# Kernel tuning notes

Hardware: AMD Instinct MI355X
Metric: run time of the kernel (lower is better)

Reference implementation:

```python
import jax, jax.numpy as jnp
import numpy as np


def setup_inputs() -> dict:
    key = jax.random.key(0)
    ks = jax.random.split(key, 5)
    B, DEC, ENC, H = 4, 256, 256, 512  # feature_dim = hl_size = 512, mlp hidden = 512
    decoder_states = jax.random.normal(ks[0], (B, DEC, H), dtype=jnp.float32)
    encoder_states = jax.random.normal(ks[1], (B, ENC, H), dtype=jnp.float32)
    ext_mask = jnp.zeros((B, DEC, ENC), dtype=bool)  # self.mask set externally; all-False here
    W_mlp = jax.random.normal(ks[2], (2 * H, H), dtype=jnp.float32) * 0.02  # Linear(2H -> H)
    b_mlp = jnp.zeros((H,), dtype=jnp.float32)
    W_out = jax.random.normal(ks[3], (H, 1), dtype=jnp.float32) * 0.02  # Linear(H -> 1)
    b_out = jnp.zeros((1,), dtype=jnp.float32)
    return {"decoder_states": decoder_states, "encoder_states": encoder_states,
            "ext_mask": ext_mask, "W_mlp": W_mlp, "b_mlp": b_mlp,
            "W_out": W_out, "b_out": b_out}


def reference(decoder_states, encoder_states, ext_mask, W_mlp, b_mlp, W_out, b_out):
    # decoder_states: [B, dec, H]; encoder_states: [B, enc, H]
    H = encoder_states.shape[-1]
    # pad mask: positions where encoder feature-0 equals 0.0 -> [B, 1, enc]
    pad_mask = (encoder_states == 0.0)[:, :, :1]
    pad_mask = jnp.swapaxes(pad_mask, 1, 2)  # [B, 1, enc]
    # cat(enc, dec) @ W_mlp  ==  enc @ W_mlp[:H] + dec @ W_mlp[H:]  (avoids 2H concat)
    enc_proj = jnp.einsum('beh,hm->bem', encoder_states, W_mlp[:H])   # [B, enc, Hm]
    dec_proj = jnp.einsum('bdh,hm->bdm', decoder_states, W_mlp[H:])   # [B, dec, Hm]
    hidden = jnp.tanh(dec_proj[:, :, None, :] + enc_proj[:, None, :, :] + b_mlp)  # [B, dec, enc, Hm]
    attn = jnp.einsum('bdem,mo->bde', hidden, W_out) + b_out[0]       # [B, dec, enc]
    attn = jnp.where(ext_mask, -jnp.inf, attn)
    attn = jnp.where(pad_mask, -jnp.inf, attn)
    attn = jax.nn.softmax(attn, axis=-1)
    context = jnp.einsum('bde,beh->bdh', attn, encoder_states)        # [B, dec, H]
    return (context, attn)
```

## Files before the change

### kernel.cpp

```cpp
#include <hip/hip_runtime.h>
#include <math.h>

#define B 4
#define DEC 256
#define ENC 256
#define HDIM 512

#define TANH_SCALE 2.8853900817779268f
#define LOG2E 1.4426950408889634f

__device__ __forceinline__ float fast_exp2(float x) { return __builtin_amdgcn_exp2f(x); }
__device__ __forceinline__ float fast_rcp(float x)  { return __builtin_amdgcn_rcpf(x); }

typedef __attribute__((ext_vector_type(8))) short bf16x8;
typedef __attribute__((ext_vector_type(4))) short bf16x4;
typedef __attribute__((ext_vector_type(4))) float f32x4;

__device__ __forceinline__ unsigned short bf16_rne(float x) {
    unsigned u = __float_as_uint(x);
    return (unsigned short)((u + 0x7FFFu + ((u >> 16) & 1u)) >> 16);
}
__device__ __forceinline__ float bf16_to_f(unsigned short h) {
    return __uint_as_float((unsigned)h << 16);
}

#define W_OFS(m, k) ((((long)(m) >> 4) << 13) + (((long)(k) >> 3) << 7) + (((m) & 15) << 3) + ((k) & 7))

__global__ __launch_bounds__(256) void convert_kernel(
    const float* __restrict__ enc, const float* __restrict__ dec,
    const float* __restrict__ Wmlp,
    unsigned short* __restrict__ Xh_e, unsigned short* __restrict__ Xl_e,
    unsigned short* __restrict__ Xh_d, unsigned short* __restrict__ Xl_d,
    unsigned short* __restrict__ Wh_e, unsigned short* __restrict__ Wl_e,
    unsigned short* __restrict__ Wh_d, unsigned short* __restrict__ Wl_d)
{
    const int tid = threadIdx.x, z = blockIdx.z;
    if (z < 2) {
        const float* X = z ? dec : enc;
        unsigned short* H = z ? Xh_d : Xh_e;
        unsigned short* L = z ? Xl_d : Xl_e;
        const long i8 = ((long)blockIdx.x * 256 + tid) * 8;
        float4 v0 = *(const float4*)(X + i8);
        float4 v1 = *(const float4*)(X + i8 + 4);
        float xs[8] = {v0.x, v0.y, v0.z, v0.w, v1.x, v1.y, v1.z, v1.w};
        bf16x8 hv, lv;
#pragma unroll
        for (int j = 0; j < 8; ++j) {
            unsigned short h = bf16_rne(xs[j]);
            hv[j] = (short)h;
            lv[j] = (short)bf16_rne(xs[j] - bf16_to_f(h));
        }
        *(bf16x8*)(H + i8) = hv;
        *(bf16x8*)(L + i8) = lv;
    } else {
        const float* Wsrc = Wmlp + (z == 3 ? (long)HDIM * HDIM : 0);
        unsigned short* H = (z == 3) ? Wh_d : Wh_e;
        unsigned short* L = (z == 3) ? Wl_d : Wl_e;
        const int t = blockIdx.x * 256 + tid;
        const int m = t & 511;
        const int k0 = (t >> 9) << 2;
        bf16x4 hv, lv;
#pragma unroll
        for (int j = 0; j < 4; ++j) {
            float x = Wsrc[(long)(k0 + j) * 512 + m];
            unsigned short h = bf16_rne(x);
            hv[j] = (short)h;
            lv[j] = (short)bf16_rne(x - bf16_to_f(h));
        }
        const long ofs = W_OFS(m, k0);
        *(bf16x4*)(H + ofs) = hv;
        *(bf16x4*)(L + ofs) = lv;
    }
}

__global__ __launch_bounds__(256) void proj_mfma_kernel(
    const unsigned short* __restrict__ Xh_e, const unsigned short* __restrict__ Xl_e,
    const unsigned short* __restrict__ Xh_d, const unsigned short* __restrict__ Xl_d,
    const unsigned short* __restrict__ Wh_e, const unsigned short* __restrict__ Wl_e,
    const unsigned short* __restrict__ Wh_d, const unsigned short* __restrict__ Wl_d,
    const float* __restrict__ bmlp,
    float* __restrict__ ET, float* __restrict__ Dmat)
{
    const int tid = threadIdx.x;
    const int wave = tid >> 6, lane = tid & 63;
    const int z = blockIdx.z;
    const int r0w = blockIdx.x * 64 + wave * 16;
    const int m0 = blockIdx.y * 32;
    const unsigned short* Xh = z ? Xh_d : Xh_e;
    const unsigned short* Xl = z ? Xl_d : Xl_e;
    const unsigned short* Wh = z ? Wh_d : Wh_e;
    const unsigned short* Wl = z ? Wl_d : Wl_e;

    const int col = lane & 15;
    const int quad = lane >> 4;

    const unsigned short* pah = Xh + (long)(r0w + col) * 512 + quad * 8;
    const unsigned short* pal = Xl + (long)(r0w + col) * 512 + quad * 8;
    const long bofs = ((long)(m0 >> 4) << 13) + (quad << 7) + (col << 3);
    const unsigned short* pb0h = Wh + bofs;
    const unsigned short* pb0l = Wl + bofs;
    const unsigned short* pb1h = Wh + bofs + 8192;
    const unsigned short* pb1l = Wl + bofs + 8192;

    f32x4 a0h = {0.f,0.f,0.f,0.f}, a0x = {0.f,0.f,0.f,0.f};
    f32x4 a1h = {0.f,0.f,0.f,0.f}, a1x = {0.f,0.f,0.f,0.f};

    bf16x8 Ah = *(const bf16x8*)pah,  Al = *(const bf16x8*)pal;
    bf16x8 B0h = *(const bf16x8*)pb0h, B0l = *(const bf16x8*)pb0l;
    bf16x8 B1h = *(const bf16x8*)pb1h, B1l = *(const bf16x8*)pb1l;

#pragma unroll 1
    for (int k0 = 0; k0 < 512; k0 += 32) {
        bf16x8 nAh = Ah, nAl = Al, nB0h = B0h, nB0l = B0l, nB1h = B1h, nB1l = B1l;
        if (k0 + 32 < 512) {
            nAh = *(const bf16x8*)(pah + k0 + 32);
            nAl = *(const bf16x8*)(pal + k0 + 32);
            const long ko = (long)(k0 + 32) << 4;
            nB0h = *(const bf16x8*)(pb0h + ko);
            nB0l = *(const bf16x8*)(pb0l + ko);
            nB1h = *(const bf16x8*)(pb1h + ko);
            nB1l = *(const bf16x8*)(pb1l + ko);
        }
        a0h = __builtin_amdgcn_mfma_f32_16x16x32_bf16(Ah, B0h, a0h, 0, 0, 0);
        a1h = __builtin_amdgcn_mfma_f32_16x16x32_bf16(Ah, B1h, a1h, 0, 0, 0);
        a0x = __builtin_amdgcn_mfma_f32_16x16x32_bf16(Ah, B0l, a0x, 0, 0, 0);
        a1x = __builtin_amdgcn_mfma_f32_16x16x32_bf16(Ah, B1l, a1x, 0, 0, 0);
        a0x = __builtin_amdgcn_mfma_f32_16x16x32_bf16(Al, B0h, a0x, 0, 0, 0);
        a1x = __builtin_amdgcn_mfma_f32_16x16x32_bf16(Al, B1h, a1x, 0, 0, 0);
        Ah = nAh; Al = nAl; B0h = nB0h; B0l = nB0l; B1h = nB1h; B1l = nB1l;
    }

    if (z == 0) {
        const int batch = r0w >> 8;
        const int e0 = (r0w & 255) + quad * 4;
        float* base = ET + (long)batch * HDIM * ENC;
        float4 v;
        v.x = fast_exp2((a0h[0] + a0x[0]) * TANH_SCALE);
        v.y = fast_exp2((a0h[1] + a0x[1]) * TANH_SCALE);
        v.z = fast_exp2((a0h[2] + a0x[2]) * TANH_SCALE);
        v.w = fast_exp2((a0h[3] + a0x[3]) * TANH_SCALE);
        *(float4*)&base[(long)(m0 + col) * ENC + e0] = v;
        v.x = fast_exp2((a1h[0] + a1x[0]) * TANH_SCALE);
        v.y = fast_exp2((a1h[1] + a1x[1]) * TANH_SCALE);
        v.z = fast_exp2((a1h[2] + a1x[2]) * TANH_SCALE);
        v.w = fast_exp2((a1h[3] + a1x[3]) * TANH_SCALE);
        *(float4*)&base[(long)(m0 + 16 + col) * ENC + e0] = v;
    } else {
        const float bq0 = bmlp[m0 + col];
        const float bq1 = bmlp[m0 + 16 + col];
        const int r = r0w + quad * 4;
#pragma unroll
        for (int i = 0; i < 4; ++i) {
            Dmat[(long)(r + i) * HDIM + m0 + col] =
                fast_exp2((a0h[i] + a0x[i] + bq0) * TANH_SCALE);
            Dmat[(long)(r + i) * HDIM + m0 + 16 + col] =
                fast_exp2((a1h[i] + a1x[i] + bq1) * TANH_SCALE);
        }
    }
}

__global__ __launch_bounds__(512) void attn_ctx_kernel(
    const float* __restrict__ Dmat, const float* __restrict__ ET,
    const float* __restrict__ wo,
    const float* __restrict__ enc, const unsigned char* __restrict__ extm,
    float* __restrict__ attn_out, float* __restrict__ ctx)
{
    __shared__ __align__(16) float ds[4][HDIM];
    __shared__ __align__(16) float wos[HDIM];
    __shared__ __align__(16) float pbuf[8][4][ENC];
    __shared__ __align__(16) float as4T[ENC][4];
    __shared__ float redm[4][4];
    __shared__ float reds[4][4];

    const int tid = threadIdx.x;
    const int b = blockIdx.z, d0 = blockIdx.x * 4;
    const long g0 = (long)b * DEC + d0;
    const int rot = blockIdx.x >> 3;

    ((float4*)ds)[tid] = ((const float4*)(Dmat + g0 * HDIM))[tid];
    if (tid < 128) ((float4*)wos)[tid] = ((const float4*)wo)[tid];

    const int mg = ((tid >> 6) + rot) & 7;
    const int e4 = (tid & 63) * 4;
    const int mbase = mg * 64;
    const float* ep = ET + (long)b * HDIM * ENC + (long)mbase * ENC + e4;

    float4 Eb0 = *(const float4*)(ep);
    float4 Eb1 = *(const float4*)(ep + ENC);
    float4 Eb2 = *(const float4*)(ep + 2 * ENC);
    float4 Eb3 = *(const float4*)(ep + 3 * ENC);
    __syncthreads();

    float acc[4][4] = {};
    for (int i = 0; i < 64; i += 2) {
        float4 Ea = Eb0, Eb = Eb1;
        Eb0 = Eb2; Eb1 = Eb3;
        if (i + 4 < 64) {
            Eb2 = *(const float4*)(ep + (long)(i + 4) * ENC);
            Eb3 = *(const float4*)(ep + (long)(i + 5) * ENC);
        }
        const int m = mbase + i;
        const float2 w2 = *(const float2*)&wos[m];
#pragma unroll
        for (int r = 0; r < 4; ++r) {
            const float2 d2 = *(const float2*)&ds[r][m];
#pragma unroll
            for (int j = 0; j < 4; ++j) {
                float ea = ((const float*)&Ea)[j];
                float eb = ((const float*)&Eb)[j];
                acc[r][j] = fmaf(w2.x, fast_rcp(fmaf(ea, d2.x, 1.0f)), acc[r][j]);
                acc[r][j] = fmaf(w2.y, fast_rcp(fmaf(eb, d2.y, 1.0f)), acc[r][j]);
            }
        }
    }
#pragma unroll
    for (int r = 0; r < 4; ++r) {
        float4 v = make_float4(acc[r][0], acc[r][1], acc[r][2], acc[r][3]);
        *(float4*)&pbuf[mg][r][e4] = v;
    }
    __syncthreads();

    const int ty = tid >> 8;
    const int e = tid & 255;
    const int wave = tid >> 6, lane = tid & 63;

    const bool pad = (enc[((long)b * ENC + e) * HDIM] == 0.0f);
    float l[2], p[2];
#pragma unroll
    for (int rl = 0; rl < 2; ++rl) {
        const int r = ty * 2 + rl;
        float a = 0.f;
#pragma unroll
        for (int q = 0; q < 8; ++q) a += pbuf[q][r][e];
        const bool xm = extm[(g0 + r) * ENC + e] != 0;
        l[rl] = (pad || xm) ? -__builtin_inff() : -2.0f * a;
    }
    float mx[2] = {l[0], l[1]};
#pragma unroll
    for (int off = 32; off >= 1; off >>= 1) {
#pragma unroll
        for (int rl = 0; rl < 2; ++rl)
            mx[rl] = fmaxf(mx[rl], __shfl_xor(mx[rl], off, 64));
    }
    if (lane == 0) {
        redm[ty * 2 + 0][wave & 3] = mx[0];
        redm[ty * 2 + 1][wave & 3] = mx[1];
    }
    __syncthreads();
    float s[2];
#pragma unroll
    for (int rl = 0; rl < 2; ++rl) {
        const int r = ty * 2 + rl;
        const float gm = fmaxf(fmaxf(redm[r][0], redm[r][1]),
                               fmaxf(redm[r][2], redm[r][3]));
        p[rl] = fast_exp2((l[rl] - gm) * LOG2E);
        s[rl] = p[rl];
    }
#pragma unroll
    for (int off = 32; off >= 1; off >>= 1) {
#pragma unroll
        for (int rl = 0; rl < 2; ++rl)
            s[rl] += __shfl_xor(s[rl], off, 64);
    }
    if (lane == 0) {
        reds[ty * 2 + 0][wave & 3] = s[0];
        reds[ty * 2 + 1][wave & 3] = s[1];
    }
    __syncthreads();
#pragma unroll
    for (int rl = 0; rl < 2; ++rl) {
        const int r = ty * 2 + rl;
        const float gs = reds[r][0] + reds[r][1] + reds[r][2] + reds[r][3];
        const float pr = p[rl] * fast_rcp(gs);
        attn_out[(g0 + r) * ENC + e] = pr;
        as4T[e][r] = pr;
    }
    __syncthreads();

    float (*p4c)[4][HDIM] = (float (*)[4][HDIM])pbuf;

    const int hq = (tid & 127) * 4;
    const int eq = ((tid >> 7) + rot) & 3;
    const int ebase = eq * 64;
    const float* ew = enc + (long)b * ENC * HDIM + (long)ebase * HDIM + hq;

    float4 Wb0 = *(const float4*)(ew);
    float4 Wb1 = *(const float4*)(ew + HDIM);
    float4 Wb2 = *(const float4*)(ew + 2 * HDIM);
    float4 Wb3 = *(const float4*)(ew + 3 * HDIM);

    float a4[4][4] = {};
    for (int i = 0; i < 64; i += 2) {
        float4 Wa = Wb0, Wc = Wb1;
        Wb0 = Wb2; Wb1 = Wb3;
        if (i + 4 < 64) {
            Wb2 = *(const float4*)(ew + (long)(i + 4) * HDIM);
            Wb3 = *(const float4*)(ew + (long)(i + 5) * HDIM);
        }
        float4 pa = *(const float4*)&as4T[ebase + i][0];
        float4 pb = *(const float4*)&as4T[ebase + i + 1][0];
#pragma unroll
        for (int r = 0; r < 4; ++r) {
            const float par = ((const float*)&pa)[r];
            const float pbr = ((const float*)&pb)[r];
#pragma unroll
            for (int j = 0; j < 4; ++j) {
                a4[r][j] = fmaf(par, ((const float*)&Wa)[j], a4[r][j]);
                a4[r][j] = fmaf(pbr, ((const float*)&Wc)[j], a4[r][j]);
            }
        }
    }
#pragma unroll
    for (int r = 0; r < 4; ++r)
        *(float4*)&p4c[eq][r][hq] = make_float4(a4[r][0], a4[r][1], a4[r][2], a4[r][3]);
    __syncthreads();

    const int h = tid;
#pragma unroll
    for (int r = 0; r < 4; ++r) {
        const float o = p4c[0][r][h] + p4c[1][r][h] + p4c[2][r][h] + p4c[3][r][h];
        ctx[(g0 + r) * HDIM + h] = o;
    }
}

extern "C" void kernel_launch(void* const* d_in, const int* in_sizes, int n_in,
                              void* d_out, int out_size, void* d_ws, size_t ws_size,
                              hipStream_t stream) {
    const float* dec = (const float*)d_in[0];
    const float* enc = (const float*)d_in[1];
    const unsigned char* extm = (const unsigned char*)d_in[2];
    const float* Wmlp = (const float*)d_in[3];
    const float* bmlp = (const float*)d_in[4];
    const float* Wout = (const float*)d_in[5];

    float* ctx = (float*)d_out;
    float* attn = ctx + (size_t)B * DEC * HDIM;

    const size_t F = (size_t)B * DEC * HDIM;
    float* ET = (float*)d_ws;
    float* Dmat = ET + F;
    unsigned short* Xh_e = (unsigned short*)(Dmat + F);
    unsigned short* Xl_e = Xh_e + F;
    unsigned short* Xh_d = Xl_e + F;
    unsigned short* Xl_d = Xh_d + F;
    unsigned short* Wh_e = Xl_d + F;
    unsigned short* Wl_e = Wh_e + HDIM * HDIM;
    unsigned short* Wh_d = Wl_e + HDIM * HDIM;
    unsigned short* Wl_d = Wh_d + HDIM * HDIM;

    convert_kernel<<<dim3(256, 1, 4), 256, 0, stream>>>(
        enc, dec, Wmlp, Xh_e, Xl_e, Xh_d, Xl_d, Wh_e, Wl_e, Wh_d, Wl_d);
    proj_mfma_kernel<<<dim3(16, 16, 2), 256, 0, stream>>>(
        Xh_e, Xl_e, Xh_d, Xl_d, Wh_e, Wl_e, Wh_d, Wl_d, bmlp, ET, Dmat);
    attn_ctx_kernel<<<dim3(DEC / 4, 1, B), 512, 0, stream>>>(
        Dmat, ET, Wout, enc, extm, attn, ctx);
}
```

Measured before the change: 110.9 us.

## Combine four reciprocals into one and deepen register prefetch in both phases

The score loop now sums four weighted reciprocals w/t over a shared denominator, so it needs one rcp per four terms plus a few extra multiplies, which cuts transcendental issue. Both the score loop and the context loop now double-buffer eight rows per thread in registers instead of four. The encoder prefetch for the context phase is hoisted above the softmax barrier so that load latency overlaps the softmax. The costs are higher register pressure and some rounding or overflow risk from the product of four denominators.

```diff
diff --git a/kernel.cpp b/kernel.cpp
--- a/kernel.cpp
+++ b/kernel.cpp
@@ -185,32 +185,46 @@
     const int mbase = mg * 64;
     const float* ep = ET + (long)b * HDIM * ENC + (long)mbase * ENC + e4;
 
-    float4 Eb0 = *(const float4*)(ep);
-    float4 Eb1 = *(const float4*)(ep + ENC);
-    float4 Eb2 = *(const float4*)(ep + 2 * ENC);
-    float4 Eb3 = *(const float4*)(ep + 3 * ENC);
+#define LDE(k) (*(const float4*)(ep + (long)(k) * ENC))
+    float4 EA0 = LDE(0), EA1 = LDE(1), EA2 = LDE(2), EA3 = LDE(3);
+    float4 EB0 = LDE(4), EB1 = LDE(5), EB2 = LDE(6), EB3 = LDE(7);
     __syncthreads();
 
     float acc[4][4] = {};
-    for (int i = 0; i < 64; i += 2) {
-        float4 Ea = Eb0, Eb = Eb1;
-        Eb0 = Eb2; Eb1 = Eb3;
-        if (i + 4 < 64) {
-            Eb2 = *(const float4*)(ep + (long)(i + 4) * ENC);
-            Eb3 = *(const float4*)(ep + (long)(i + 5) * ENC);
-        }
-        const int m = mbase + i;
-        const float2 w2 = *(const float2*)&wos[m];
-#pragma unroll
-        for (int r = 0; r < 4; ++r) {
-            const float2 d2 = *(const float2*)&ds[r][m];
-#pragma unroll
-            for (int j = 0; j < 4; ++j) {
-                float ea = ((const float*)&Ea)[j];
-                float eb = ((const float*)&Eb)[j];
-                acc[r][j] = fmaf(w2.x, fast_rcp(fmaf(ea, d2.x, 1.0f)), acc[r][j]);
-                acc[r][j] = fmaf(w2.y, fast_rcp(fmaf(eb, d2.y, 1.0f)), acc[r][j]);
-            }
+
+#define PH2_QUAD(C0, C1, C2, C3, M)                                          \
+    {                                                                        \
+        const float4 w4 = *(const float4*)&wos[(M)];                         \
+        _Pragma("unroll")                                                    \
+        for (int r = 0; r < 4; ++r) {                                        \
+            const float4 d4 = *(const float4*)&ds[r][(M)];                   \
+            _Pragma("unroll")                                                \
+            for (int j = 0; j < 4; ++j) {                                    \
+                const float t0 = fmaf(((const float*)&C0)[j], d4.x, 1.0f);   \
+                const float t1 = fmaf(((const float*)&C1)[j], d4.y, 1.0f);   \
+                const float t2 = fmaf(((const float*)&C2)[j], d4.z, 1.0f);   \
+                const float t3 = fmaf(((const float*)&C3)[j], d4.w, 1.0f);   \
+                const float p01 = t0 * t1;                                   \
+                const float p23 = t2 * t3;                                   \
+                const float n01 = fmaf(w4.x, t1, w4.y * t0);                 \
+                const float n23 = fmaf(w4.z, t3, w4.w * t2);                 \
+                const float N = fmaf(n01, p23, n23 * p01);                   \
+                acc[r][j] = fmaf(N, fast_rcp(p01 * p23), acc[r][j]);         \
+            }                                                                \
+        }                                                                    \
+    }
+
+#pragma unroll 1
+    for (int i = 0; i < 64; i += 8) {
+        PH2_QUAD(EA0, EA1, EA2, EA3, mbase + i)
+        if (i + 8 < 64) {
+            EA0 = LDE(i + 8);  EA1 = LDE(i + 9);
+            EA2 = LDE(i + 10); EA3 = LDE(i + 11);
+        }
+        PH2_QUAD(EB0, EB1, EB2, EB3, mbase + i + 4)
+        if (i + 8 < 64) {
+            EB0 = LDE(i + 12); EB1 = LDE(i + 13);
+            EB2 = LDE(i + 14); EB3 = LDE(i + 15);
         }
     }
 #pragma unroll
@@ -218,6 +232,15 @@
         float4 v = make_float4(acc[r][0], acc[r][1], acc[r][2], acc[r][3]);
         *(float4*)&pbuf[mg][r][e4] = v;
     }
+
+    const int hq = (tid & 127) * 4;
+    const int eq = ((tid >> 7) + rot) & 3;
+    const int ebase = eq * 64;
+    const float* ew = enc + (long)b * ENC * HDIM + (long)ebase * HDIM + hq;
+#define LDW(k) (*(const float4*)(ew + (long)(k) * HDIM))
+    float4 WA0 = LDW(0), WA1 = LDW(1), WA2 = LDW(2), WA3 = LDW(3);
+    float4 WB0 = LDW(4), WB1 = LDW(5), WB2 = LDW(6), WB3 = LDW(7);
+
     __syncthreads();
 
     const int ty = tid >> 8;
@@ -279,35 +302,41 @@
 
     float (*p4c)[4][HDIM] = (float (*)[4][HDIM])pbuf;
 
-    const int hq = (tid & 127) * 4;
-    const int eq = ((tid >> 7) + rot) & 3;
-    const int ebase = eq * 64;
-    const float* ew = enc + (long)b * ENC * HDIM + (long)ebase * HDIM + hq;
-
-    float4 Wb0 = *(const float4*)(ew);
-    float4 Wb1 = *(const float4*)(ew + HDIM);
-    float4 Wb2 = *(const float4*)(ew + 2 * HDIM);
-    float4 Wb3 = *(const float4*)(ew + 3 * HDIM);
-
     float a4[4][4] = {};
-    for (int i = 0; i < 64; i += 2) {
-        float4 Wa = Wb0, Wc = Wb1;
-        Wb0 = Wb2; Wb1 = Wb3;
-        if (i + 4 < 64) {
-            Wb2 = *(const float4*)(ew + (long)(i + 4) * HDIM);
-            Wb3 = *(const float4*)(ew + (long)(i + 5) * HDIM);
-        }
-        float4 pa = *(const float4*)&as4T[ebase + i][0];
-        float4 pb = *(const float4*)&as4T[ebase + i + 1][0];
-#pragma unroll
-        for (int r = 0; r < 4; ++r) {
-            const float par = ((const float*)&pa)[r];
-            const float pbr = ((const float*)&pb)[r];
-#pragma unroll
-            for (int j = 0; j < 4; ++j) {
-                a4[r][j] = fmaf(par, ((const float*)&Wa)[j], a4[r][j]);
-                a4[r][j] = fmaf(pbr, ((const float*)&Wc)[j], a4[r][j]);
-            }
+
+#define PH4_QUAD(C0, C1, C2, C3, E0)                                         \
+    {                                                                        \
+        const float4 pa = *(const float4*)&as4T[(E0) + 0][0];                \
+        const float4 pb = *(const float4*)&as4T[(E0) + 1][0];                \
+        const float4 pc = *(const float4*)&as4T[(E0) + 2][0];                \
+        const float4 pd = *(const float4*)&as4T[(E0) + 3][0];                \
+        _Pragma("unroll")                                                    \
+        for (int r = 0; r < 4; ++r) {                                        \
+            const float par = ((const float*)&pa)[r];                        \
+            const float pbr = ((const float*)&pb)[r];                        \
+            const float pcr = ((const float*)&pc)[r];                        \
+            const float pdr = ((const float*)&pd)[r];                        \
+            _Pragma("unroll")                                                \
+            for (int j = 0; j < 4; ++j) {                                    \
+                a4[r][j] = fmaf(par, ((const float*)&C0)[j], a4[r][j]);      \
+                a4[r][j] = fmaf(pbr, ((const float*)&C1)[j], a4[r][j]);      \
+                a4[r][j] = fmaf(pcr, ((const float*)&C2)[j], a4[r][j]);      \
+                a4[r][j] = fmaf(pdr, ((const float*)&C3)[j], a4[r][j]);      \
+            }                                                                \
+        }                                                                    \
+    }
+
+#pragma unroll 1
+    for (int i = 0; i < 64; i += 8) {
+        PH4_QUAD(WA0, WA1, WA2, WA3, ebase + i)
+        if (i + 8 < 64) {
+            WA0 = LDW(i + 8);  WA1 = LDW(i + 9);
+            WA2 = LDW(i + 10); WA3 = LDW(i + 11);
+        }
+        PH4_QUAD(WB0, WB1, WB2, WB3, ebase + i + 4)
+        if (i + 8 < 64) {
+            WB0 = LDW(i + 12); WB1 = LDW(i + 13);
+            WB2 = LDW(i + 14); WB3 = LDW(i + 15);
         }
     }
 #pragma unroll
```

Result: faster. 104.0 us (-6.2%).
